# Kernel tuning notes

Hardware: AMD Instinct MI355X
Metric: run time of the kernel (lower is better)

The kernel has to match this reference:

```python
import jax, jax.numpy as jnp
import numpy as np

# --- static config (matches init_kwargs) ---
T, V, D, H = 4096, 32000, 1024, 16
DH = D // H                      # rope/head dim = 64
E, CAP, K, HOPS = 8, 1024, 2, 3  # non-identity experts, capacity, top-k, hops
MLP = 4 * D
ROPE_BASE = 10000.0
ATTN_IDX = np.array([0, 2, 4, 6])  # experts built with i%2==0 -> Attention
FFN_IDX = np.array([1, 3, 5, 7])   # i%2==1 -> FeedForward
EPS = 1e-6


def rope_cos_sin(t, dh, base):
    inv = 1.0 / (base ** (jnp.arange(0, dh, 2, dtype=jnp.float32) / dh))
    ang = jnp.arange(t, dtype=jnp.float32)[:, None] * inv[None, :]  # [T, dh/2]
    ang = jnp.concatenate([ang, ang], axis=-1)                      # [T, dh]
    return jnp.cos(ang), jnp.sin(ang)


def rotate_half(x):
    h = x.shape[-1] // 2
    return jnp.concatenate([-x[..., h:], x[..., :h]], axis=-1)


def topk_mask(logits, k):
    # boolean [T, E_total] mask of per-row top-k
    _, idx = jax.lax.top_k(logits, k)
    hard = jax.nn.one_hot(idx, logits.shape[-1]).sum(axis=-2)
    return hard.astype(bool)


def capacity_select(mask_te, gate_te, capacity):
    # mask_te: [T,E] bool, gate_te: [T,E] float -> slot [E,C,T], kept [E,T]
    m = mask_te.T                                   # [E, T]
    g = jnp.where(m, gate_te.T, -jnp.inf)           # [E, T]
    cap = int(min(capacity, g.shape[1]))
    _, top_idx = jax.lax.top_k(g, cap)              # [E, C]
    Ee, C = top_idx.shape
    slot = jnp.zeros((Ee, C, g.shape[1]), g.dtype)
    slot = slot.at[jnp.arange(Ee)[:, None], jnp.arange(C)[None, :], top_idx].set(1.0)
    slot = slot * m[:, None, :]                     # drop -inf fill slots
    kept = slot.sum(1).astype(bool)                 # [E, T]
    return slot, kept


def rms_norm(x, w):
    return x * jax.lax.rsqrt(jnp.mean(x * x, axis=-1, keepdims=True) + EPS) * w


def attention_group(x, cos_r, sin_r, wq, wk, wv, wo):
    # x: [G,C,D]; cos_r/sin_r: [G,C,DH]; weights: [G,D,D]
    G, C, _ = x.shape
    q = jnp.einsum('gcd,gde->gce', x, wq).reshape(G, C, H, DH)
    k = jnp.einsum('gcd,gde->gce', x, wk).reshape(G, C, H, DH)
    v = jnp.einsum('gcd,gde->gce', x, wv).reshape(G, C, H, DH)
    c = cos_r[:, :, None, :]
    s = sin_r[:, :, None, :]
    q = q * c + rotate_half(q) * s
    k = k * c + rotate_half(k) * s
    scores = jnp.einsum('gqhd,gkhd->ghqk', q, k) / np.sqrt(DH).astype(np.float32)
    attn = jax.nn.softmax(scores, axis=-1)
    out = jnp.einsum('ghqk,gkhd->gqhd', attn, v).reshape(G, C, D)
    return jnp.einsum('gcd,gde->gce', out, wo)


def ffn_group(x, w1, w2):
    # x: [G,C,D]; w1: [G,D,MLP]; w2: [G,MLP,D]
    return jnp.einsum('gcf,gfd->gcd', jax.nn.gelu(jnp.einsum('gcd,gdf->gcf', x, w1)), w2)


def dna_forward(ids, embed_w, router_w, wq, wk, wv, wo, w1, w2, ln_w):
    h = embed_w[ids]                                     # [T, D]
    cos, sin = rope_cos_sin(T, DH, ROPE_BASE)            # [T, DH]
    for hop in range(HOPS):
        logits = h @ router_w[hop].T                     # [T, E+1]
        probs = jax.nn.softmax(logits, axis=-1)
        mask_full = topk_mask(logits, K)                 # [T, E+1]
        probs_tr = probs[:, :-1]                         # [T, E]
        mask_tr = mask_full[:, :-1]
        slot, kept = capacity_select(mask_tr, probs_tr, CAP)  # [E,C,T], [E,T]
        # dispatch
        xin = jnp.einsum('ect,td->ecd', slot, h)          # [E, C, D]
        cos_r = jnp.einsum('ect,td->ecd', slot, cos)      # [E, C, DH]
        sin_r = jnp.einsum('ect,td->ecd', slot, sin)
        # grouped expert execution (stacked params, vectorized over group dim)
        attn_out = attention_group(xin[ATTN_IDX], cos_r[ATTN_IDX], sin_r[ATTN_IDX],
                                   wq, wk, wv, wo)        # [4, C, D]
        ffn_out = ffn_group(xin[FFN_IDX], w1, w2)         # [4, C, D]
        expert_out = jnp.zeros((E, CAP, D), h.dtype)
        expert_out = expert_out.at[ATTN_IDX].set(attn_out).at[FFN_IDX].set(ffn_out)
        # combine
        combine_w = jnp.where(kept.T, probs_tr, 0.0)      # [T, E]
        rho = combine_w.sum(axis=1, keepdims=True)        # [T, 1]
        combine = jnp.einsum('ecd,ect,et->td', expert_out, slot, combine_w.T)
        h = h + combine - rho * h
    return rms_norm(h, ln_w)


def setup_inputs() -> dict:
    key = jax.random.key(0)
    ks = jax.random.split(key, 10)
    sc = 0.02
    return {
        'ids': jax.random.randint(ks[0], (T,), 0, V),
        'embed_w': jax.random.normal(ks[1], (V, D), jnp.float32) * sc,
        'router_w': jax.random.normal(ks[2], (HOPS, E + 1, D), jnp.float32) * sc,
        'wq': jax.random.normal(ks[3], (4, D, D), jnp.float32) * sc,
        'wk': jax.random.normal(ks[4], (4, D, D), jnp.float32) * sc,
        'wv': jax.random.normal(ks[5], (4, D, D), jnp.float32) * sc,
        'wo': jax.random.normal(ks[6], (4, D, D), jnp.float32) * sc,
        'w1': jax.random.normal(ks[7], (4, D, MLP), jnp.float32) * sc,
        'w2': jax.random.normal(ks[8], (4, MLP, D), jnp.float32) * sc,
        'ln_w': jnp.ones((D,), jnp.float32),
    }


def reference(ids, embed_w, router_w, wq, wk, wv, wo, w1, w2, ln_w):
    return dna_forward(ids, embed_w, router_w, wq, wk, wv, wo, w1, w2, ln_w)
```

## Files before the change

### kernel.cpp

```cpp
#include <hip/hip_runtime.h>
#include <math.h>

#define T_ 4096
#define D_ 1024
#define H_ 16
#define DH_ 64
#define E_ 8
#define CAP_ 1024
#define MLP_ 4096
#define HOPS_ 3

__global__ __launch_bounds__(256) void embed_kernel(
    const int* __restrict__ ids, const float* __restrict__ ew, float* __restrict__ h)
{
  const int t = blockIdx.x;
  const int id = ids[t];
  const int c = threadIdx.x * 4;
  *(float4*)(h + (size_t)t * D_ + c) = *(const float4*)(ew + (size_t)id * D_ + c);
}

__global__ __launch_bounds__(64) void router_kernel(
    const float* __restrict__ h, const float* __restrict__ rw,
    float* __restrict__ probs, float* __restrict__ gmask)
{
  const int t = blockIdx.x;
  const int lane = threadIdx.x;
  __shared__ float hs[D_];
  #pragma unroll
  for (int j = 0; j < 4; ++j)
    *(float4*)&hs[lane * 4 + j * 256] = *(const float4*)(h + (size_t)t * D_ + lane * 4 + j * 256);
  __syncthreads();
  float l9[9];
  #pragma unroll
  for (int e = 0; e < 9; ++e) {
    float s = 0.0f;
    for (int i = lane; i < D_; i += 64) s += hs[i] * rw[e * D_ + i];
    #pragma unroll
    for (int off = 32; off > 0; off >>= 1) s += __shfl_down(s, off);
    l9[e] = s;
  }
  if (lane == 0) {
    float m = l9[0];
    #pragma unroll
    for (int e = 1; e < 9; ++e) m = fmaxf(m, l9[e]);
    float sum = 0.0f;
    float ex[9];
    #pragma unroll
    for (int e = 0; e < 9; ++e) { ex[e] = expf(l9[e] - m); sum += ex[e]; }
    const float inv = 1.0f / sum;
    int b1 = 0;
    #pragma unroll
    for (int e = 1; e < 9; ++e) if (l9[e] > l9[b1]) b1 = e;
    int b2 = (b1 == 0) ? 1 : 0;
    #pragma unroll
    for (int e = 0; e < 9; ++e) if (e != b1 && e != b2 && l9[e] > l9[b2]) b2 = e;
    #pragma unroll
    for (int e = 0; e < 8; ++e) {
      const float pe = ex[e] * inv;
      probs[t * 8 + e] = pe;
      gmask[(size_t)e * T_ + t] = (e == b1 || e == b2) ? pe : -1e30f;
    }
  }
}

__global__ __launch_bounds__(256) void zero_kernel(float* __restrict__ rho, int* __restrict__ cnt)
{
  const int i = blockIdx.x * 256 + threadIdx.x;
  if (i < T_) rho[i] = 0.0f;
  if (i < E_) cnt[i] = 0;
}

__global__ __launch_bounds__(256) void select_kernel(
    const float* __restrict__ gmask, const float* __restrict__ probs,
    int* __restrict__ idx, int* __restrict__ cnt, float* __restrict__ rho)
{
  __shared__ float row[T_];
  const int e = blockIdx.y;
  const int tid = threadIdx.x;
  const float* gr = gmask + (size_t)e * T_;
  #pragma unroll
  for (int j = 0; j < 16; ++j) row[tid + 256 * j] = gr[tid + 256 * j];
  __syncthreads();
  const int t = blockIdx.x * 256 + tid;
  const float g = row[t];
  if (g > -1e29f) {
    int rank = 0;
    for (int tt = 0; tt < T_; ++tt) {
      const float gg = row[tt];
      rank += (gg > g) || (gg == g && tt < t);
    }
    if (rank < CAP_) {
      const int pos = atomicAdd(&cnt[e], 1);
      idx[e * CAP_ + pos] = t;
      atomicAdd(&rho[t], probs[t * 8 + e]);
    }
  }
}

__global__ __launch_bounds__(256) void gather_kernel(
    const float* __restrict__ h, const int* __restrict__ idx, const int* __restrict__ cnt,
    float* __restrict__ xin)
{
  const int c = blockIdx.x, e = blockIdx.y;
  const int c4 = threadIdx.x * 4;
  float4* dst = (float4*)(xin + ((size_t)e * CAP_ + c) * D_ + c4);
  if (c < cnt[e]) {
    const int t = idx[e * CAP_ + c];
    *dst = *(const float4*)(h + (size_t)t * D_ + c4);
  } else {
    float4 z; z.x = z.y = z.z = z.w = 0.0f;
    *dst = z;
  }
}

typedef __bf16 bf16x8 __attribute__((ext_vector_type(8)));
typedef float f32x4v __attribute__((ext_vector_type(4)));

union FragU { uint2 u2[2]; bf16x8 v; };

__device__ __forceinline__ unsigned pack_hi2(unsigned u0, unsigned u1)
{
  return (u0 >> 16) | (u1 & 0xFFFF0000u);
}

__device__ __forceinline__ void split8(const float4 a, const float4 b, FragU& h, FragU& l)
{
  const float f[8] = {a.x, a.y, a.z, a.w, b.x, b.y, b.z, b.w};
  unsigned hu[8], lu[8];
  #pragma unroll
  for (int i = 0; i < 8; ++i) {
    const unsigned u = __float_as_uint(f[i]);
    const float lo = f[i] - __uint_as_float(u & 0xFFFF0000u);
    hu[i] = u; lu[i] = __float_as_uint(lo);
  }
  h.u2[0].x = pack_hi2(hu[0], hu[1]); h.u2[0].y = pack_hi2(hu[2], hu[3]);
  h.u2[1].x = pack_hi2(hu[4], hu[5]); h.u2[1].y = pack_hi2(hu[6], hu[7]);
  l.u2[0].x = pack_hi2(lu[0], lu[1]); l.u2[0].y = pack_hi2(lu[2], lu[3]);
  l.u2[1].x = pack_hi2(lu[4], lu[5]); l.u2[1].y = pack_hi2(lu[6], lu[7]);
}

#define BM 128
#define BN 128
#define BK 32
#define LDT 36

__device__ __forceinline__ float gelu_tanh(float x)
{
  const float x3 = x * x * x;
  return 0.5f * x * (1.0f + tanhf(0.7978845608028654f * (x + 0.044715f * x3)));
}

template <int EPI>
__device__ __forceinline__ void gemm_core(
    const float* __restrict__ A, const float* __restrict__ B, float* __restrict__ C,
    int N, int K)
{
  __shared__ unsigned short Ah[BM * LDT];
  __shared__ unsigned short Al[BM * LDT];
  __shared__ unsigned short Bh[BN * LDT];
  __shared__ unsigned short Bl[BN * LDT];

  const int tid = threadIdx.x;
  const int lane = tid & 63;
  const int w = tid >> 6;
  const int wm = w >> 1, wn = w & 1;
  const int m0 = blockIdx.y * BM;
  const int n0 = blockIdx.x * BN;
  const int q = lane >> 4;
  const int l15 = lane & 15;

  const int a_mo = tid >> 3;
  const int a_kq = (tid & 7) * 4;
  const int b_n = tid & 127;
  const int b_kh = (tid >> 7) * 16;

  f32x4v acc[4][4];
  #pragma unroll
  for (int i = 0; i < 4; ++i)
    #pragma unroll
    for (int j = 0; j < 4; ++j) { acc[i][j][0] = 0.f; acc[i][j][1] = 0.f; acc[i][j][2] = 0.f; acc[i][j][3] = 0.f; }

  float4 a_reg[4];
  float b_reg[16];

  const int nk = K / BK;
  #pragma unroll
  for (int t = 0; t < 4; ++t)
    a_reg[t] = *(const float4*)(A + (size_t)(m0 + t * 32 + a_mo) * K + a_kq);
  {
    const float* Bp = B + (size_t)b_kh * N + n0 + b_n;
    #pragma unroll
    for (int i = 0; i < 16; ++i) b_reg[i] = Bp[(size_t)i * N];
  }

  for (int kt = 0; kt < nk; ++kt) {
    __syncthreads();
    #pragma unroll
    for (int t = 0; t < 4; ++t) {
      const int m = t * 32 + a_mo;
      const unsigned u0 = __float_as_uint(a_reg[t].x);
      const unsigned u1 = __float_as_uint(a_reg[t].y);
      const unsigned u2 = __float_as_uint(a_reg[t].z);
      const unsigned u3 = __float_as_uint(a_reg[t].w);
      const float l0 = a_reg[t].x - __uint_as_float(u0 & 0xFFFF0000u);
      const float l1 = a_reg[t].y - __uint_as_float(u1 & 0xFFFF0000u);
      const float l2 = a_reg[t].z - __uint_as_float(u2 & 0xFFFF0000u);
      const float l3 = a_reg[t].w - __uint_as_float(u3 & 0xFFFF0000u);
      uint2 hp, lp;
      hp.x = pack_hi2(u0, u1); hp.y = pack_hi2(u2, u3);
      lp.x = pack_hi2(__float_as_uint(l0), __float_as_uint(l1));
      lp.y = pack_hi2(__float_as_uint(l2), __float_as_uint(l3));
      *(uint2*)&Ah[m * LDT + a_kq] = hp;
      *(uint2*)&Al[m * LDT + a_kq] = lp;
    }
    #pragma unroll
    for (int i = 0; i < 4; ++i) {
      const float f0 = b_reg[4 * i + 0], f1 = b_reg[4 * i + 1];
      const float f2 = b_reg[4 * i + 2], f3 = b_reg[4 * i + 3];
      const unsigned u0 = __float_as_uint(f0);
      const unsigned u1 = __float_as_uint(f1);
      const unsigned u2 = __float_as_uint(f2);
      const unsigned u3 = __float_as_uint(f3);
      const float l0 = f0 - __uint_as_float(u0 & 0xFFFF0000u);
      const float l1 = f1 - __uint_as_float(u1 & 0xFFFF0000u);
      const float l2 = f2 - __uint_as_float(u2 & 0xFFFF0000u);
      const float l3 = f3 - __uint_as_float(u3 & 0xFFFF0000u);
      uint2 hp, lp;
      hp.x = pack_hi2(u0, u1); hp.y = pack_hi2(u2, u3);
      lp.x = pack_hi2(__float_as_uint(l0), __float_as_uint(l1));
      lp.y = pack_hi2(__float_as_uint(l2), __float_as_uint(l3));
      *(uint2*)&Bh[b_n * LDT + b_kh + 4 * i] = hp;
      *(uint2*)&Bl[b_n * LDT + b_kh + 4 * i] = lp;
    }
    if (kt + 1 < nk) {
      const int k0 = (kt + 1) * BK;
      #pragma unroll
      for (int t = 0; t < 4; ++t)
        a_reg[t] = *(const float4*)(A + (size_t)(m0 + t * 32 + a_mo) * K + k0 + a_kq);
      const float* Bp = B + (size_t)(k0 + b_kh) * N + n0 + b_n;
      #pragma unroll
      for (int i = 0; i < 16; ++i) b_reg[i] = Bp[(size_t)i * N];
    }
    __syncthreads();
    FragU fa_h[4], fa_l[4], fb_h[4], fb_l[4];
    #pragma unroll
    for (int i = 0; i < 4; ++i) {
      const int m = wm * 64 + i * 16 + l15;
      const unsigned short* pa = &Ah[m * LDT + q * 8];
      const unsigned short* pl = &Al[m * LDT + q * 8];
      fa_h[i].u2[0] = *(const uint2*)pa; fa_h[i].u2[1] = *(const uint2*)(pa + 4);
      fa_l[i].u2[0] = *(const uint2*)pl; fa_l[i].u2[1] = *(const uint2*)(pl + 4);
    }
    #pragma unroll
    for (int j = 0; j < 4; ++j) {
      const int n = wn * 64 + j * 16 + l15;
      const unsigned short* pb = &Bh[n * LDT + q * 8];
      const unsigned short* pl = &Bl[n * LDT + q * 8];
      fb_h[j].u2[0] = *(const uint2*)pb; fb_h[j].u2[1] = *(const uint2*)(pb + 4);
      fb_l[j].u2[0] = *(const uint2*)pl; fb_l[j].u2[1] = *(const uint2*)(pl + 4);
    }
    #pragma unroll
    for (int i = 0; i < 4; ++i)
      #pragma unroll
      for (int j = 0; j < 4; ++j) {
        acc[i][j] = __builtin_amdgcn_mfma_f32_16x16x32_bf16(fa_h[i].v, fb_h[j].v, acc[i][j], 0, 0, 0);
        acc[i][j] = __builtin_amdgcn_mfma_f32_16x16x32_bf16(fa_h[i].v, fb_l[j].v, acc[i][j], 0, 0, 0);
        acc[i][j] = __builtin_amdgcn_mfma_f32_16x16x32_bf16(fa_l[i].v, fb_h[j].v, acc[i][j], 0, 0, 0);
      }
  }
  #pragma unroll
  for (int i = 0; i < 4; ++i)
    #pragma unroll
    for (int j = 0; j < 4; ++j) {
      const int n = n0 + wn * 64 + j * 16 + l15;
      #pragma unroll
      for (int r = 0; r < 4; ++r) {
        const int m = m0 + wm * 64 + i * 16 + q * 4 + r;
        float v = acc[i][j][r];
        if (EPI == 1) v = gelu_tanh(v);
        C[(size_t)m * N + n] = v;
      }
    }
}

template <int EPI>
__global__ __launch_bounds__(256, 2) void gemm_split(
    const float* __restrict__ Abase, const float* __restrict__ Bbase, float* __restrict__ Cbase,
    int N, int K, long sA, long sB, long sC)
{
  const float* A = Abase + (size_t)blockIdx.z * (size_t)sA;
  const float* B = Bbase + (size_t)blockIdx.z * (size_t)sB;
  float* C = Cbase + (size_t)blockIdx.z * (size_t)sC;
  gemm_core<EPI>(A, B, C, N, K);
}

__global__ __launch_bounds__(256, 2) void gemm_qkv(
    const float* __restrict__ xin,
    const float* __restrict__ wq, const float* __restrict__ wk, const float* __restrict__ wv,
    float* __restrict__ qb, float* __restrict__ kb, float* __restrict__ vb)
{
  const int z = blockIdx.z;
  const int g = z & 3;
  const int which = z >> 2;
  const float* A = xin + (size_t)g * 2 * CAP_ * D_;
  const float* B = ((which == 0) ? wq : (which == 1) ? wk : wv) + (size_t)g * D_ * D_;
  float* C = ((which == 0) ? qb : (which == 1) ? kb : vb) + (size_t)g * CAP_ * D_;
  gemm_core<0>(A, B, C, D_, D_);
}

__global__ __launch_bounds__(256) void rope_kernel(
    float* __restrict__ q, float* __restrict__ k,
    const int* __restrict__ idx, const int* __restrict__ cnt)
{
  const int c = blockIdx.x, g = blockIdx.y;
  const int e = 2 * g;
  if (c >= cnt[e]) return;
  const int t = idx[e * CAP_ + c];
  const int tid = threadIdx.x;
  const int hh = tid >> 4;
  const int pp = tid & 15;
  const size_t base = ((size_t)g * CAP_ + c) * D_ + hh * DH_;
  const float tf = (float)t;
  #pragma unroll
  for (int u = 0; u < 2; ++u) {
    const int i = pp * 2 + u;
    const float invf = (float)::pow(10000.0, -(double)i / 32.0);
    const float ang = tf * invf;
    const float cs = (float)::cos((double)ang);
    const float sn = (float)::sin((double)ang);
    const float q0 = q[base + i], q1 = q[base + i + 32];
    q[base + i]      = q0 * cs - q1 * sn;
    q[base + i + 32] = q1 * cs + q0 * sn;
    const float k0 = k[base + i], k1 = k[base + i + 32];
    k[base + i]      = k0 * cs - k1 * sn;
    k[base + i + 32] = k1 * cs + k0 * sn;
  }
}

#define FBQ 128
#define LDK 68
#define LDQ 72

__global__ __launch_bounds__(256, 2) void flash_mfma(
    const float* __restrict__ qg, const float* __restrict__ kg,
    const float* __restrict__ vg, float* __restrict__ og)
{
  const int g = blockIdx.z, hh = blockIdx.y, qt = blockIdx.x;
  const size_t base = (size_t)g * CAP_ * D_ + hh * DH_;
  const float* Q = qg + base;
  const float* Kp = kg + base;
  const float* Vp = vg + base;
  float* O = og + base;

  __shared__ __align__(16) char lds_raw[69632];
  unsigned short* Kh  = (unsigned short*)lds_raw;
  unsigned short* Kl  = Kh  + 64 * LDK;
  unsigned short* Vth = Kl  + 64 * LDK;
  unsigned short* Vtl = Vth + 64 * LDK;
  unsigned short* Ph  = Vtl + 64 * LDK;
  unsigned short* Pl  = Ph  + FBQ * LDK;
  float* Qs = (float*)lds_raw;

  const int tid = threadIdx.x;
  const int lane = tid & 63;
  const int w = tid >> 6;
  const int quad = lane >> 4;
  const int l15 = lane & 15;

  #pragma unroll
  for (int it = 0; it < 8; ++it) {
    const int row = it * 16 + (tid >> 4);
    const int c4 = (tid & 15) * 4;
    *(float4*)&Qs[row * LDQ + c4] = *(const float4*)(Q + (size_t)(qt * FBQ + row) * D_ + c4);
  }
  __syncthreads();
  FragU qf[2][2][2];
  #pragma unroll
  for (int rs = 0; rs < 2; ++rs)
    #pragma unroll
    for (int ks = 0; ks < 2; ++ks) {
      const float* p0 = &Qs[(w * 32 + rs * 16 + l15) * LDQ + ks * 32 + quad * 8];
      const float4 f0 = *(const float4*)p0;
      const float4 f1 = *(const float4*)(p0 + 4);
      split8(f0, f1, qf[rs][ks][0], qf[rs][ks][1]);
    }
  __syncthreads();

  f32x4v acc[2][4];
  float m_r[2][4], l_r[2][4];
  #pragma unroll
  for (int rs = 0; rs < 2; ++rs)
    #pragma unroll
    for (int r = 0; r < 4; ++r) { m_r[rs][r] = -1e30f; l_r[rs][r] = 0.0f; }
  #pragma unroll
  for (int rs = 0; rs < 2; ++rs)
    #pragma unroll
    for (int dt = 0; dt < 4; ++dt) { acc[rs][dt][0] = 0.f; acc[rs][dt][1] = 0.f; acc[rs][dt][2] = 0.f; acc[rs][dt][3] = 0.f; }

  for (int kt = 0; kt < 16; ++kt) {
    __syncthreads();
    #pragma unroll
    for (int it = 0; it < 4; ++it) {
      const int r = it * 16 + (tid >> 4);
      const int c4 = (tid & 15) * 4;
      const float4 kv = *(const float4*)(Kp + (size_t)(kt * 64 + r) * D_ + c4);
      {
        const unsigned u0 = __float_as_uint(kv.x), u1 = __float_as_uint(kv.y);
        const unsigned u2 = __float_as_uint(kv.z), u3 = __float_as_uint(kv.w);
        const float l0 = kv.x - __uint_as_float(u0 & 0xFFFF0000u);
        const float l1 = kv.y - __uint_as_float(u1 & 0xFFFF0000u);
        const float l2 = kv.z - __uint_as_float(u2 & 0xFFFF0000u);
        const float l3 = kv.w - __uint_as_float(u3 & 0xFFFF0000u);
        uint2 hp, lp;
        hp.x = pack_hi2(u0, u1); hp.y = pack_hi2(u2, u3);
        lp.x = pack_hi2(__float_as_uint(l0), __float_as_uint(l1));
        lp.y = pack_hi2(__float_as_uint(l2), __float_as_uint(l3));
        *(uint2*)&Kh[r * LDK + c4] = hp;
        *(uint2*)&Kl[r * LDK + c4] = lp;
      }
      const float4 vv = *(const float4*)(Vp + (size_t)(kt * 64 + r) * D_ + c4);
      const float vf[4] = {vv.x, vv.y, vv.z, vv.w};
      #pragma unroll
      for (int u = 0; u < 4; ++u) {
        const unsigned uu = __float_as_uint(vf[u]);
        const float lo = vf[u] - __uint_as_float(uu & 0xFFFF0000u);
        Vth[(c4 + u) * LDK + r] = (unsigned short)(uu >> 16);
        Vtl[(c4 + u) * LDK + r] = (unsigned short)(__float_as_uint(lo) >> 16);
      }
    }
    __syncthreads();
    f32x4v sfr[2][4];
    #pragma unroll
    for (int rs = 0; rs < 2; ++rs)
      #pragma unroll
      for (int j = 0; j < 4; ++j) {
        f32x4v s; s[0] = 0.f; s[1] = 0.f; s[2] = 0.f; s[3] = 0.f;
        #pragma unroll
        for (int ks = 0; ks < 2; ++ks) {
          FragU kh, kl;
          const unsigned short* pk = &Kh[(j * 16 + l15) * LDK + ks * 32 + quad * 8];
          const unsigned short* pl = &Kl[(j * 16 + l15) * LDK + ks * 32 + quad * 8];
          kh.u2[0] = *(const uint2*)pk; kh.u2[1] = *(const uint2*)(pk + 4);
          kl.u2[0] = *(const uint2*)pl; kl.u2[1] = *(const uint2*)(pl + 4);
          s = __builtin_amdgcn_mfma_f32_16x16x32_bf16(qf[rs][ks][0].v, kh.v, s, 0, 0, 0);
          s = __builtin_amdgcn_mfma_f32_16x16x32_bf16(qf[rs][ks][0].v, kl.v, s, 0, 0, 0);
          s = __builtin_amdgcn_mfma_f32_16x16x32_bf16(qf[rs][ks][1].v, kh.v, s, 0, 0, 0);
        }
        sfr[rs][j] = s;
      }
    #pragma unroll
    for (int rs = 0; rs < 2; ++rs) {
      #pragma unroll
      for (int r = 0; r < 4; ++r) {
        float s0 = sfr[rs][0][r] * 0.125f;
        float s1 = sfr[rs][1][r] * 0.125f;
        float s2 = sfr[rs][2][r] * 0.125f;
        float s3 = sfr[rs][3][r] * 0.125f;
        float mx = fmaxf(fmaxf(s0, s1), fmaxf(s2, s3));
        #pragma unroll
        for (int o = 1; o < 16; o <<= 1) mx = fmaxf(mx, __shfl_xor(mx, o));
        const float nm = fmaxf(m_r[rs][r], mx);
        const float al = __expf(m_r[rs][r] - nm);
        m_r[rs][r] = nm;
        const float p0 = __expf(s0 - nm);
        const float p1 = __expf(s1 - nm);
        const float p2 = __expf(s2 - nm);
        const float p3 = __expf(s3 - nm);
        float rsum = p0 + p1 + p2 + p3;
        #pragma unroll
        for (int o = 1; o < 16; o <<= 1) rsum += __shfl_xor(rsum, o);
        l_r[rs][r] = l_r[rs][r] * al + rsum;
        #pragma unroll
        for (int dt = 0; dt < 4; ++dt) acc[rs][dt][r] *= al;
        const int row = w * 32 + rs * 16 + quad * 4 + r;
        const float pv[4] = {p0, p1, p2, p3};
        #pragma unroll
        for (int j = 0; j < 4; ++j) {
          const unsigned u = __float_as_uint(pv[j]);
          const float lo = pv[j] - __uint_as_float(u & 0xFFFF0000u);
          Ph[row * LDK + j * 16 + l15] = (unsigned short)(u >> 16);
          Pl[row * LDK + j * 16 + l15] = (unsigned short)(__float_as_uint(lo) >> 16);
        }
      }
    }
    __syncthreads();
    FragU pf[2][2][2];
    #pragma unroll
    for (int rs = 0; rs < 2; ++rs)
      #pragma unroll
      for (int ks = 0; ks < 2; ++ks) {
        const unsigned short* ph = &Ph[(w * 32 + rs * 16 + l15) * LDK + ks * 32 + quad * 8];
        const unsigned short* pl = &Pl[(w * 32 + rs * 16 + l15) * LDK + ks * 32 + quad * 8];
        pf[rs][ks][0].u2[0] = *(const uint2*)ph; pf[rs][ks][0].u2[1] = *(const uint2*)(ph + 4);
        pf[rs][ks][1].u2[0] = *(const uint2*)pl; pf[rs][ks][1].u2[1] = *(const uint2*)(pl + 4);
      }
    #pragma unroll
    for (int dt = 0; dt < 4; ++dt)
      #pragma unroll
      for (int ks = 0; ks < 2; ++ks) {
        FragU vh, vl;
        const unsigned short* pv_ = &Vth[(dt * 16 + l15) * LDK + ks * 32 + quad * 8];
        const unsigned short* pl_ = &Vtl[(dt * 16 + l15) * LDK + ks * 32 + quad * 8];
        vh.u2[0] = *(const uint2*)pv_; vh.u2[1] = *(const uint2*)(pv_ + 4);
        vl.u2[0] = *(const uint2*)pl_; vl.u2[1] = *(const uint2*)(pl_ + 4);
        #pragma unroll
        for (int rs = 0; rs < 2; ++rs) {
          acc[rs][dt] = __builtin_amdgcn_mfma_f32_16x16x32_bf16(pf[rs][ks][0].v, vh.v, acc[rs][dt], 0, 0, 0);
          acc[rs][dt] = __builtin_amdgcn_mfma_f32_16x16x32_bf16(pf[rs][ks][0].v, vl.v, acc[rs][dt], 0, 0, 0);
          acc[rs][dt] = __builtin_amdgcn_mfma_f32_16x16x32_bf16(pf[rs][ks][1].v, vh.v, acc[rs][dt], 0, 0, 0);
        }
      }
  }
  #pragma unroll
  for (int rs = 0; rs < 2; ++rs)
    #pragma unroll
    for (int r = 0; r < 4; ++r) {
      const float inv = 1.0f / l_r[rs][r];
      const int row = qt * FBQ + w * 32 + rs * 16 + quad * 4 + r;
      #pragma unroll
      for (int dt = 0; dt < 4; ++dt)
        O[(size_t)row * D_ + dt * 16 + l15] = acc[rs][dt][r] * inv;
    }
}

__global__ __launch_bounds__(256) void initnew_kernel(
    const float* __restrict__ h, const float* __restrict__ rho, float* __restrict__ hn)
{
  const int t = blockIdx.x;
  const float f = 1.0f - rho[t];
  const int c = threadIdx.x * 4;
  float4 x = *(const float4*)(h + (size_t)t * D_ + c);
  x.x *= f; x.y *= f; x.z *= f; x.w *= f;
  *(float4*)(hn + (size_t)t * D_ + c) = x;
}

__global__ __launch_bounds__(256) void scatter_kernel(
    const float* __restrict__ eo, const int* __restrict__ idx, const int* __restrict__ cnt,
    const float* __restrict__ probs, float* __restrict__ hn)
{
  const int c = blockIdx.x, e = blockIdx.y;
  if (c >= cnt[e]) return;
  const int t = idx[e * CAP_ + c];
  const float w = probs[t * 8 + e];
  const float* src = eo + ((size_t)e * CAP_ + c) * D_;
  float* dst = hn + (size_t)t * D_;
  const int c4 = threadIdx.x * 4;
  #pragma unroll
  for (int j = 0; j < 4; ++j) atomicAdd(dst + c4 + j, src[c4 + j] * w);
}

__global__ __launch_bounds__(256) void rms_kernel(
    const float* __restrict__ h, const float* __restrict__ w, float* __restrict__ out)
{
  const int t = blockIdx.x;
  const int c = threadIdx.x * 4;
  const float4 x = *(const float4*)(h + (size_t)t * D_ + c);
  float ss = x.x * x.x + x.y * x.y + x.z * x.z + x.w * x.w;
  #pragma unroll
  for (int off = 32; off > 0; off >>= 1) ss += __shfl_down(ss, off);
  __shared__ float wsum[4];
  __shared__ float sscale;
  const int lane = threadIdx.x & 63, wv = threadIdx.x >> 6;
  if (lane == 0) wsum[wv] = ss;
  __syncthreads();
  if (threadIdx.x == 0) {
    const float s = wsum[0] + wsum[1] + wsum[2] + wsum[3];
    sscale = 1.0f / sqrtf(s * (1.0f / (float)D_) + 1e-6f);
  }
  __syncthreads();
  const float sc = sscale;
  const float4 w4 = *(const float4*)(w + c);
  float4 o;
  o.x = x.x * sc * w4.x; o.y = x.y * sc * w4.y; o.z = x.z * sc * w4.z; o.w = x.w * sc * w4.w;
  *(float4*)(out + (size_t)t * D_ + c) = o;
}

extern "C" void kernel_launch(void* const* d_in, const int* in_sizes, int n_in,
                              void* d_out, int out_size, void* d_ws, size_t ws_size,
                              hipStream_t stream)
{
  (void)in_sizes; (void)n_in; (void)out_size; (void)ws_size;
  const int* ids = (const int*)d_in[0];
  const float* embed_w = (const float*)d_in[1];
  const float* router_w = (const float*)d_in[2];
  const float* wq = (const float*)d_in[3];
  const float* wk = (const float*)d_in[4];
  const float* wv = (const float*)d_in[5];
  const float* wo = (const float*)d_in[6];
  const float* w1 = (const float*)d_in[7];
  const float* w2 = (const float*)d_in[8];
  const float* lnw = (const float*)d_in[9];
  float* out = (float*)d_out;

  float* p = (float*)d_ws;
  const size_t TD = (size_t)T_ * D_;
  float* hA = p;    p += TD;
  float* hB = p;    p += TD;
  float* probs = p; p += (size_t)T_ * E_;
  float* gmask = p; p += (size_t)E_ * T_;
  float* rho = p;   p += T_;
  int* idx = (int*)p;   p += E_ * CAP_;
  int* cnt = (int*)p;   p += 16;
  float* xin = p;  p += (size_t)E_ * CAP_ * D_;
  float* qb = p;   p += (size_t)4 * CAP_ * D_;
  float* kb = p;   p += (size_t)4 * CAP_ * D_;
  float* vb = p;   p += (size_t)4 * CAP_ * D_;
  float* ao = p;   p += (size_t)4 * CAP_ * D_;
  float* eo = p;   p += (size_t)E_ * CAP_ * D_;
  float* mid = qb;

  embed_kernel<<<T_, 256, 0, stream>>>(ids, embed_w, hA);
  float* cur = hA;
  float* nxt = hB;
  for (int hop = 0; hop < HOPS_; ++hop) {
    router_kernel<<<T_, 64, 0, stream>>>(cur, router_w + (size_t)hop * 9 * D_, probs, gmask);
    zero_kernel<<<16, 256, 0, stream>>>(rho, cnt);
    select_kernel<<<dim3(16, 8), 256, 0, stream>>>(gmask, probs, idx, cnt, rho);
    gather_kernel<<<dim3(CAP_, E_), 256, 0, stream>>>(cur, idx, cnt, xin);
    gemm_qkv<<<dim3(D_ / BN, CAP_ / BM, 12), 256, 0, stream>>>(xin, wq, wk, wv, qb, kb, vb);
    rope_kernel<<<dim3(CAP_, 4), 256, 0, stream>>>(qb, kb, idx, cnt);
    flash_mfma<<<dim3(CAP_ / FBQ, 16, 4), 256, 0, stream>>>(qb, kb, vb, ao);
    gemm_split<0><<<dim3(D_ / BN, CAP_ / BM, 4), 256, 0, stream>>>(
        ao, wo, eo, D_, D_,
        (long)CAP_ * D_, (long)D_ * D_, (long)2 * CAP_ * D_);
    gemm_split<1><<<dim3(MLP_ / BN, CAP_ / BM, 4), 256, 0, stream>>>(
        xin + (size_t)CAP_ * D_, w1, mid, MLP_, D_,
        (long)2 * CAP_ * D_, (long)D_ * MLP_, (long)CAP_ * MLP_);
    gemm_split<0><<<dim3(D_ / BN, CAP_ / BM, 4), 256, 0, stream>>>(
        mid, w2, eo + (size_t)CAP_ * D_, D_, MLP_,
        (long)CAP_ * MLP_, (long)MLP_ * D_, (long)2 * CAP_ * D_);
    initnew_kernel<<<T_, 256, 0, stream>>>(cur, rho, nxt);
    scatter_kernel<<<dim3(CAP_, E_), 256, 0, stream>>>(eo, idx, cnt, probs, nxt);
    float* tmp = cur; cur = nxt; nxt = tmp;
  }
  rms_kernel<<<T_, 256, 0, stream>>>(cur, lnw, out);
}
```

Measured before the change: 2.758 ms.

## Pre-split operands into bf16 hi/lo layout and use direct-to-LDS GEMM loads

Weights are converted once per call into transposed bf16 hi/lo split buffers. Activations (gathered inputs, attention output, GELU output) are written directly in the same split layout. The GEMM core no longer splits fp32 values in its inner loop; it streams pre-split tiles via global_load_lds and runs the three hi/lo product phases as separate K-steps. The wo and w2 GEMMs use split-K with atomicAdd into a zeroed buffer to add parallelism, at the cost of extra conversion passes, atomics, and more workspace.

```diff
diff --git a/kernel.cpp b/kernel.cpp
--- a/kernel.cpp
+++ b/kernel.cpp
@@ -68,6 +68,13 @@
   const int i = blockIdx.x * 256 + threadIdx.x;
   if (i < T_) rho[i] = 0.0f;
   if (i < E_) cnt[i] = 0;
+}
+
+__global__ __launch_bounds__(256) void zeroeo_kernel(float* __restrict__ eo)
+{
+  const size_t i = ((size_t)blockIdx.x * 256 + threadIdx.x) * 4;
+  float4 z; z.x = z.y = z.z = z.w = 0.0f;
+  *(float4*)(eo + i) = z;
 }
 
 __global__ __launch_bounds__(256) void select_kernel(
@@ -97,22 +104,6 @@
   }
 }
 
-__global__ __launch_bounds__(256) void gather_kernel(
-    const float* __restrict__ h, const int* __restrict__ idx, const int* __restrict__ cnt,
-    float* __restrict__ xin)
-{
-  const int c = blockIdx.x, e = blockIdx.y;
-  const int c4 = threadIdx.x * 4;
-  float4* dst = (float4*)(xin + ((size_t)e * CAP_ + c) * D_ + c4);
-  if (c < cnt[e]) {
-    const int t = idx[e * CAP_ + c];
-    *dst = *(const float4*)(h + (size_t)t * D_ + c4);
-  } else {
-    float4 z; z.x = z.y = z.z = z.w = 0.0f;
-    *dst = z;
-  }
-}
-
 typedef __bf16 bf16x8 __attribute__((ext_vector_type(8)));
 typedef float f32x4v __attribute__((ext_vector_type(4)));
 
@@ -139,10 +130,12 @@
   l.u2[1].x = pack_hi2(lu[4], lu[5]); l.u2[1].y = pack_hi2(lu[6], lu[7]);
 }
 
-#define BM 128
-#define BN 128
-#define BK 32
-#define LDT 36
+__device__ __forceinline__ void lds_load16(const void* g, void* l)
+{
+  __builtin_amdgcn_global_load_lds(
+      (const __attribute__((address_space(1))) unsigned int*)g,
+      (__attribute__((address_space(3))) unsigned int*)l, 16, 0, 0);
+}
 
 __device__ __forceinline__ float gelu_tanh(float x)
 {
@@ -150,29 +143,77 @@
   return 0.5f * x * (1.0f + tanhf(0.7978845608028654f * (x + 0.044715f * x3)));
 }
 
+__global__ __launch_bounds__(256) void gather_kernel(
+    const float* __restrict__ h, const int* __restrict__ idx, const int* __restrict__ cnt,
+    unsigned short* __restrict__ xinp)
+{
+  const int c = blockIdx.x, e = blockIdx.y;
+  const int c4 = threadIdx.x * 4;
+  unsigned short* dst = xinp + ((size_t)e * CAP_ + c) * 2 * D_;
+  if (c < cnt[e]) {
+    const int t = idx[e * CAP_ + c];
+    const float4 x = *(const float4*)(h + (size_t)t * D_ + c4);
+    const float f[4] = {x.x, x.y, x.z, x.w};
+    unsigned hu[4], lu[4];
+    #pragma unroll
+    for (int j = 0; j < 4; ++j) {
+      const unsigned u = __float_as_uint(f[j]);
+      const float lo = f[j] - __uint_as_float(u & 0xFFFF0000u);
+      hu[j] = u; lu[j] = __float_as_uint(lo);
+    }
+    uint2 hp, lp;
+    hp.x = pack_hi2(hu[0], hu[1]); hp.y = pack_hi2(hu[2], hu[3]);
+    lp.x = pack_hi2(lu[0], lu[1]); lp.y = pack_hi2(lu[2], lu[3]);
+    *(uint2*)(dst + c4) = hp;
+    *(uint2*)(dst + D_ + c4) = lp;
+  } else {
+    uint2 z; z.x = 0u; z.y = 0u;
+    *(uint2*)(dst + c4) = z;
+    *(uint2*)(dst + D_ + c4) = z;
+  }
+}
+
+__global__ __launch_bounds__(256) void convw_kernel(
+    const float* __restrict__ W, unsigned short* __restrict__ out, int K, int N)
+{
+  const float* Wp = W + (size_t)blockIdx.z * K * N;
+  unsigned short* op = out + (size_t)blockIdx.z * N * 2 * K;
+  const int k0 = blockIdx.y * 64, n0 = blockIdx.x * 64;
+  __shared__ float tile[64][65];
+  const int tr = threadIdx.x >> 6;
+  const int tc = threadIdx.x & 63;
+  #pragma unroll
+  for (int it = 0; it < 16; ++it) {
+    const int r = it * 4 + tr;
+    tile[r][tc] = Wp[(size_t)(k0 + r) * N + n0 + tc];
+  }
+  __syncthreads();
+  #pragma unroll
+  for (int it = 0; it < 16; ++it) {
+    const int n = it * 4 + tr;
+    const float f = tile[tc][n];
+    const unsigned u = __float_as_uint(f);
+    const float lo = f - __uint_as_float(u & 0xFFFF0000u);
+    op[(size_t)(n0 + n) * 2 * K + k0 + tc] = (unsigned short)(u >> 16);
+    op[(size_t)(n0 + n) * 2 * K + K + k0 + tc] = (unsigned short)(__float_as_uint(lo) >> 16);
+  }
+}
+
 template <int EPI>
-__device__ __forceinline__ void gemm_core(
-    const float* __restrict__ A, const float* __restrict__ B, float* __restrict__ C,
-    int N, int K)
-{
-  __shared__ unsigned short Ah[BM * LDT];
-  __shared__ unsigned short Al[BM * LDT];
-  __shared__ unsigned short Bh[BN * LDT];
-  __shared__ unsigned short Bl[BN * LDT];
+__device__ __forceinline__ void gemm_bf16_core(
+    const unsigned short* __restrict__ A, const unsigned short* __restrict__ B,
+    void* __restrict__ Cv, int N, int K, int vt0, int nvt)
+{
+  __shared__ unsigned short As[128 * 64];
+  __shared__ unsigned short Bs[128 * 64];
 
   const int tid = threadIdx.x;
   const int lane = tid & 63;
   const int w = tid >> 6;
   const int wm = w >> 1, wn = w & 1;
-  const int m0 = blockIdx.y * BM;
-  const int n0 = blockIdx.x * BN;
-  const int q = lane >> 4;
-  const int l15 = lane & 15;
-
-  const int a_mo = tid >> 3;
-  const int a_kq = (tid & 7) * 4;
-  const int b_n = tid & 127;
-  const int b_kh = (tid >> 7) * 16;
+  const int quad = lane >> 4, l15 = lane & 15;
+  const int m0 = blockIdx.y * 128, n0 = blockIdx.x * 128;
+  const size_t K2 = (size_t)2 * K;
 
   f32x4v acc[4][4];
   #pragma unroll
@@ -180,94 +221,45 @@
     #pragma unroll
     for (int j = 0; j < 4; ++j) { acc[i][j][0] = 0.f; acc[i][j][1] = 0.f; acc[i][j][2] = 0.f; acc[i][j][3] = 0.f; }
 
-  float4 a_reg[4];
-  float b_reg[16];
-
-  const int nk = K / BK;
-  #pragma unroll
-  for (int t = 0; t < 4; ++t)
-    a_reg[t] = *(const float4*)(A + (size_t)(m0 + t * 32 + a_mo) * K + a_kq);
-  {
-    const float* Bp = B + (size_t)b_kh * N + n0 + b_n;
-    #pragma unroll
-    for (int i = 0; i < 16; ++i) b_reg[i] = Bp[(size_t)i * N];
-  }
-
-  for (int kt = 0; kt < nk; ++kt) {
+  const int r0 = tid >> 3;
+  const int c0 = (tid & 7) * 8;
+
+  for (int vt = vt0; vt < vt0 + nvt; ++vt) {
+    const int kk = vt / 3;
+    const int ph = vt - kk * 3;
+    const int ka = kk * 64 + (ph == 2 ? K : 0);
+    const int kb = kk * 64 + (ph == 1 ? K : 0);
     __syncthreads();
-    #pragma unroll
-    for (int t = 0; t < 4; ++t) {
-      const int m = t * 32 + a_mo;
-      const unsigned u0 = __float_as_uint(a_reg[t].x);
-      const unsigned u1 = __float_as_uint(a_reg[t].y);
-      const unsigned u2 = __float_as_uint(a_reg[t].z);
-      const unsigned u3 = __float_as_uint(a_reg[t].w);
-      const float l0 = a_reg[t].x - __uint_as_float(u0 & 0xFFFF0000u);
-      const float l1 = a_reg[t].y - __uint_as_float(u1 & 0xFFFF0000u);
-      const float l2 = a_reg[t].z - __uint_as_float(u2 & 0xFFFF0000u);
-      const float l3 = a_reg[t].w - __uint_as_float(u3 & 0xFFFF0000u);
-      uint2 hp, lp;
-      hp.x = pack_hi2(u0, u1); hp.y = pack_hi2(u2, u3);
-      lp.x = pack_hi2(__float_as_uint(l0), __float_as_uint(l1));
-      lp.y = pack_hi2(__float_as_uint(l2), __float_as_uint(l3));
-      *(uint2*)&Ah[m * LDT + a_kq] = hp;
-      *(uint2*)&Al[m * LDT + a_kq] = lp;
-    }
-    #pragma unroll
-    for (int i = 0; i < 4; ++i) {
-      const float f0 = b_reg[4 * i + 0], f1 = b_reg[4 * i + 1];
-      const float f2 = b_reg[4 * i + 2], f3 = b_reg[4 * i + 3];
-      const unsigned u0 = __float_as_uint(f0);
-      const unsigned u1 = __float_as_uint(f1);
-      const unsigned u2 = __float_as_uint(f2);
-      const unsigned u3 = __float_as_uint(f3);
-      const float l0 = f0 - __uint_as_float(u0 & 0xFFFF0000u);
-      const float l1 = f1 - __uint_as_float(u1 & 0xFFFF0000u);
-      const float l2 = f2 - __uint_as_float(u2 & 0xFFFF0000u);
-      const float l3 = f3 - __uint_as_float(u3 & 0xFFFF0000u);
-      uint2 hp, lp;
-      hp.x = pack_hi2(u0, u1); hp.y = pack_hi2(u2, u3);
-      lp.x = pack_hi2(__float_as_uint(l0), __float_as_uint(l1));
-      lp.y = pack_hi2(__float_as_uint(l2), __float_as_uint(l3));
-      *(uint2*)&Bh[b_n * LDT + b_kh + 4 * i] = hp;
-      *(uint2*)&Bl[b_n * LDT + b_kh + 4 * i] = lp;
-    }
-    if (kt + 1 < nk) {
-      const int k0 = (kt + 1) * BK;
-      #pragma unroll
-      for (int t = 0; t < 4; ++t)
-        a_reg[t] = *(const float4*)(A + (size_t)(m0 + t * 32 + a_mo) * K + k0 + a_kq);
-      const float* Bp = B + (size_t)(k0 + b_kh) * N + n0 + b_n;
-      #pragma unroll
-      for (int i = 0; i < 16; ++i) b_reg[i] = Bp[(size_t)i * N];
-    }
+    const unsigned short* Ag = A + (size_t)(m0 + r0) * K2 + ka + c0;
+    const unsigned short* Bg = B + (size_t)(n0 + r0) * K2 + kb + c0;
+    #pragma unroll
+    for (int i = 0; i < 4; ++i)
+      lds_load16(Ag + (size_t)(i * 32) * K2, &As[(tid + i * 256) * 8]);
+    #pragma unroll
+    for (int i = 0; i < 4; ++i)
+      lds_load16(Bg + (size_t)(i * 32) * K2, &Bs[(tid + i * 256) * 8]);
     __syncthreads();
-    FragU fa_h[4], fa_l[4], fb_h[4], fb_l[4];
-    #pragma unroll
-    for (int i = 0; i < 4; ++i) {
-      const int m = wm * 64 + i * 16 + l15;
-      const unsigned short* pa = &Ah[m * LDT + q * 8];
-      const unsigned short* pl = &Al[m * LDT + q * 8];
-      fa_h[i].u2[0] = *(const uint2*)pa; fa_h[i].u2[1] = *(const uint2*)(pa + 4);
-      fa_l[i].u2[0] = *(const uint2*)pl; fa_l[i].u2[1] = *(const uint2*)(pl + 4);
-    }
-    #pragma unroll
-    for (int j = 0; j < 4; ++j) {
-      const int n = wn * 64 + j * 16 + l15;
-      const unsigned short* pb = &Bh[n * LDT + q * 8];
-      const unsigned short* pl = &Bl[n * LDT + q * 8];
-      fb_h[j].u2[0] = *(const uint2*)pb; fb_h[j].u2[1] = *(const uint2*)(pb + 4);
-      fb_l[j].u2[0] = *(const uint2*)pl; fb_l[j].u2[1] = *(const uint2*)(pl + 4);
-    }
-    #pragma unroll
-    for (int i = 0; i < 4; ++i)
+    #pragma unroll
+    for (int ks = 0; ks < 2; ++ks) {
+      FragU fa[4], fb[4];
+      #pragma unroll
+      for (int i = 0; i < 4; ++i) {
+        const unsigned short* pa = &As[(wm * 64 + i * 16 + l15) * 64 + ks * 32 + quad * 8];
+        fa[i].u2[0] = *(const uint2*)pa; fa[i].u2[1] = *(const uint2*)(pa + 4);
+      }
       #pragma unroll
       for (int j = 0; j < 4; ++j) {
-        acc[i][j] = __builtin_amdgcn_mfma_f32_16x16x32_bf16(fa_h[i].v, fb_h[j].v, acc[i][j], 0, 0, 0);
-        acc[i][j] = __builtin_amdgcn_mfma_f32_16x16x32_bf16(fa_h[i].v, fb_l[j].v, acc[i][j], 0, 0, 0);
-        acc[i][j] = __builtin_amdgcn_mfma_f32_16x16x32_bf16(fa_l[i].v, fb_h[j].v, acc[i][j], 0, 0, 0);
-      }
-  }
+        const unsigned short* pb = &Bs[(wn * 64 + j * 16 + l15) * 64 + ks * 32 + quad * 8];
+        fb[j].u2[0] = *(const uint2*)pb; fb[j].u2[1] = *(const uint2*)(pb + 4);
+      }
+      #pragma unroll
+      for (int i = 0; i < 4; ++i)
+        #pragma unroll
+        for (int j = 0; j < 4; ++j)
+          acc[i][j] = __builtin_amdgcn_mfma_f32_16x16x32_bf16(fa[i].v, fb[j].v, acc[i][j], 0, 0, 0);
+    }
+  }
+
   #pragma unroll
   for (int i = 0; i < 4; ++i)
     #pragma unroll
@@ -275,37 +267,54 @@
       const int n = n0 + wn * 64 + j * 16 + l15;
       #pragma unroll
       for (int r = 0; r < 4; ++r) {
-        const int m = m0 + wm * 64 + i * 16 + q * 4 + r;
-        float v = acc[i][j][r];
-        if (EPI == 1) v = gelu_tanh(v);
-        C[(size_t)m * N + n] = v;
-      }
-    }
-}
-
-template <int EPI>
-__global__ __launch_bounds__(256, 2) void gemm_split(
-    const float* __restrict__ Abase, const float* __restrict__ Bbase, float* __restrict__ Cbase,
-    int N, int K, long sA, long sB, long sC)
-{
-  const float* A = Abase + (size_t)blockIdx.z * (size_t)sA;
-  const float* B = Bbase + (size_t)blockIdx.z * (size_t)sB;
-  float* C = Cbase + (size_t)blockIdx.z * (size_t)sC;
-  gemm_core<EPI>(A, B, C, N, K);
-}
-
-__global__ __launch_bounds__(256, 2) void gemm_qkv(
-    const float* __restrict__ xin,
-    const float* __restrict__ wq, const float* __restrict__ wk, const float* __restrict__ wv,
+        const int m = m0 + wm * 64 + i * 16 + quad * 4 + r;
+        const float v = acc[i][j][r];
+        if (EPI == 0) {
+          ((float*)Cv)[(size_t)m * N + n] = v;
+        } else if (EPI == 2) {
+          atomicAdd(&((float*)Cv)[(size_t)m * N + n], v);
+        } else {
+          const float gv = gelu_tanh(v);
+          const unsigned u = __float_as_uint(gv);
+          const float lo = gv - __uint_as_float(u & 0xFFFF0000u);
+          unsigned short* C = (unsigned short*)Cv;
+          C[(size_t)m * 2 * N + n] = (unsigned short)(u >> 16);
+          C[(size_t)m * 2 * N + N + n] = (unsigned short)(__float_as_uint(lo) >> 16);
+        }
+      }
+    }
+}
+
+template <int EPI, int SK>
+__global__ __launch_bounds__(256, 2) void gemm_bf16_k(
+    const unsigned short* __restrict__ Ab, const unsigned short* __restrict__ Bb,
+    void* __restrict__ Cb, int N, int K, long sA, long sB, long sC)
+{
+  const int z = blockIdx.z;
+  const int g = z / SK, sp = z - g * SK;
+  const unsigned short* A = Ab + (size_t)g * sA;
+  const unsigned short* B = Bb + (size_t)g * sB;
+  void* C;
+  if (EPI == 1) C = (void*)((unsigned short*)Cb + (size_t)g * sC);
+  else          C = (void*)((float*)Cb + (size_t)g * sC);
+  const int kps = K / 64;
+  const int per = 3 * kps / SK;
+  gemm_bf16_core<EPI>(A, B, C, N, K, sp * per, per);
+}
+
+__global__ __launch_bounds__(256, 2) void gemm_qkv_bf16(
+    const unsigned short* __restrict__ xinp,
+    const unsigned short* __restrict__ wqp, const unsigned short* __restrict__ wkp,
+    const unsigned short* __restrict__ wvp,
     float* __restrict__ qb, float* __restrict__ kb, float* __restrict__ vb)
 {
   const int z = blockIdx.z;
   const int g = z & 3;
   const int which = z >> 2;
-  const float* A = xin + (size_t)g * 2 * CAP_ * D_;
-  const float* B = ((which == 0) ? wq : (which == 1) ? wk : wv) + (size_t)g * D_ * D_;
+  const unsigned short* A = xinp + (size_t)(2 * g) * CAP_ * 2 * D_;
+  const unsigned short* B = ((which == 0) ? wqp : (which == 1) ? wkp : wvp) + (size_t)g * D_ * 2 * D_;
   float* C = ((which == 0) ? qb : (which == 1) ? kb : vb) + (size_t)g * CAP_ * D_;
-  gemm_core<0>(A, B, C, D_, D_);
+  gemm_bf16_core<0>(A, B, (void*)C, D_, D_, 0, 48);
 }
 
 __global__ __launch_bounds__(256) void rope_kernel(
@@ -343,14 +352,14 @@
 
 __global__ __launch_bounds__(256, 2) void flash_mfma(
     const float* __restrict__ qg, const float* __restrict__ kg,
-    const float* __restrict__ vg, float* __restrict__ og)
+    const float* __restrict__ vg, unsigned short* __restrict__ og)
 {
   const int g = blockIdx.z, hh = blockIdx.y, qt = blockIdx.x;
   const size_t base = (size_t)g * CAP_ * D_ + hh * DH_;
   const float* Q = qg + base;
   const float* Kp = kg + base;
   const float* Vp = vg + base;
-  float* O = og + base;
+  unsigned short* Ob = og + (size_t)g * CAP_ * 2 * D_ + hh * DH_;
 
   __shared__ __align__(16) char lds_raw[69632];
   unsigned short* Kh  = (unsigned short*)lds_raw;
@@ -518,8 +527,13 @@
       const float inv = 1.0f / l_r[rs][r];
       const int row = qt * FBQ + w * 32 + rs * 16 + quad * 4 + r;
       #pragma unroll
-      for (int dt = 0; dt < 4; ++dt)
-        O[(size_t)row * D_ + dt * 16 + l15] = acc[rs][dt][r] * inv;
+      for (int dt = 0; dt < 4; ++dt) {
+        const float v = acc[rs][dt][r] * inv;
+        const unsigned u = __float_as_uint(v);
+        const float lo = v - __uint_as_float(u & 0xFFFF0000u);
+        Ob[(size_t)row * 2 * D_ + dt * 16 + l15] = (unsigned short)(u >> 16);
+        Ob[(size_t)row * 2 * D_ + D_ + dt * 16 + l15] = (unsigned short)(__float_as_uint(lo) >> 16);
+      }
     }
 }
 
@@ -601,13 +615,26 @@
   float* rho = p;   p += T_;
   int* idx = (int*)p;   p += E_ * CAP_;
   int* cnt = (int*)p;   p += 16;
-  float* xin = p;  p += (size_t)E_ * CAP_ * D_;
+  float* eo = p;   p += (size_t)E_ * CAP_ * D_;
   float* qb = p;   p += (size_t)4 * CAP_ * D_;
   float* kb = p;   p += (size_t)4 * CAP_ * D_;
   float* vb = p;   p += (size_t)4 * CAP_ * D_;
-  float* ao = p;   p += (size_t)4 * CAP_ * D_;
-  float* eo = p;   p += (size_t)E_ * CAP_ * D_;
-  float* mid = qb;
+  unsigned short* aob = (unsigned short*)p; p += (size_t)4 * CAP_ * D_;
+  unsigned short* midp = (unsigned short*)qb;
+  unsigned short* xinp = (unsigned short*)p; p += (size_t)E_ * CAP_ * D_;
+  unsigned short* wqp = (unsigned short*)p; p += (size_t)4 * D_ * D_;
+  unsigned short* wkp = (unsigned short*)p; p += (size_t)4 * D_ * D_;
+  unsigned short* wvp = (unsigned short*)p; p += (size_t)4 * D_ * D_;
+  unsigned short* wop = (unsigned short*)p; p += (size_t)4 * D_ * D_;
+  unsigned short* w1p = (unsigned short*)p; p += (size_t)4 * D_ * MLP_;
+  unsigned short* w2p = (unsigned short*)p; p += (size_t)4 * D_ * MLP_;
+
+  convw_kernel<<<dim3(D_ / 64, D_ / 64, 4), 256, 0, stream>>>(wq, wqp, D_, D_);
+  convw_kernel<<<dim3(D_ / 64, D_ / 64, 4), 256, 0, stream>>>(wk, wkp, D_, D_);
+  convw_kernel<<<dim3(D_ / 64, D_ / 64, 4), 256, 0, stream>>>(wv, wvp, D_, D_);
+  convw_kernel<<<dim3(D_ / 64, D_ / 64, 4), 256, 0, stream>>>(wo, wop, D_, D_);
+  convw_kernel<<<dim3(MLP_ / 64, D_ / 64, 4), 256, 0, stream>>>(w1, w1p, D_, MLP_);
+  convw_kernel<<<dim3(D_ / 64, MLP_ / 64, 4), 256, 0, stream>>>(w2, w2p, MLP_, D_);
 
   embed_kernel<<<T_, 256, 0, stream>>>(ids, embed_w, hA);
   float* cur = hA;
@@ -616,19 +643,20 @@
     router_kernel<<<T_, 64, 0, stream>>>(cur, router_w + (size_t)hop * 9 * D_, probs, gmask);
     zero_kernel<<<16, 256, 0, stream>>>(rho, cnt);
     select_kernel<<<dim3(16, 8), 256, 0, stream>>>(gmask, probs, idx, cnt, rho);
-    gather_kernel<<<dim3(CAP_, E_), 256, 0, stream>>>(cur, idx, cnt, xin);
-    gemm_qkv<<<dim3(D_ / BN, CAP_ / BM, 12), 256, 0, stream>>>(xin, wq, wk, wv, qb, kb, vb);
+    gather_kernel<<<dim3(CAP_, E_), 256, 0, stream>>>(cur, idx, cnt, xinp);
+    gemm_qkv_bf16<<<dim3(D_ / 128, CAP_ / 128, 12), 256, 0, stream>>>(xinp, wqp, wkp, wvp, qb, kb, vb);
     rope_kernel<<<dim3(CAP_, 4), 256, 0, stream>>>(qb, kb, idx, cnt);
-    flash_mfma<<<dim3(CAP_ / FBQ, 16, 4), 256, 0, stream>>>(qb, kb, vb, ao);
-    gemm_split<0><<<dim3(D_ / BN, CAP_ / BM, 4), 256, 0, stream>>>(
-        ao, wo, eo, D_, D_,
-        (long)CAP_ * D_, (long)D_ * D_, (long)2 * CAP_ * D_);
-    gemm_split<1><<<dim3(MLP_ / BN, CAP_ / BM, 4), 256, 0, stream>>>(
-        xin + (size_t)CAP_ * D_, w1, mid, MLP_, D_,
-        (long)2 * CAP_ * D_, (long)D_ * MLP_, (long)CAP_ * MLP_);
-    gemm_split<0><<<dim3(D_ / BN, CAP_ / BM, 4), 256, 0, stream>>>(
-        mid, w2, eo + (size_t)CAP_ * D_, D_, MLP_,
-        (long)CAP_ * MLP_, (long)MLP_ * D_, (long)2 * CAP_ * D_);
+    flash_mfma<<<dim3(CAP_ / FBQ, 16, 4), 256, 0, stream>>>(qb, kb, vb, aob);
+    zeroeo_kernel<<<8192, 256, 0, stream>>>(eo);
+    gemm_bf16_k<2, 4><<<dim3(D_ / 128, CAP_ / 128, 16), 256, 0, stream>>>(
+        aob, wop, (void*)eo, D_, D_,
+        (long)CAP_ * 2 * D_, (long)D_ * 2 * D_, (long)2 * CAP_ * D_);
+    gemm_bf16_k<1, 1><<<dim3(MLP_ / 128, CAP_ / 128, 4), 256, 0, stream>>>(
+        xinp + (size_t)CAP_ * 2 * D_, w1p, (void*)midp, MLP_, D_,
+        (long)2 * CAP_ * 2 * D_, (long)MLP_ * 2 * D_, (long)CAP_ * 2 * MLP_);
+    gemm_bf16_k<2, 4><<<dim3(D_ / 128, CAP_ / 128, 16), 256, 0, stream>>>(
+        midp, w2p, (void*)(eo + (size_t)CAP_ * D_), D_, MLP_,
+        (long)CAP_ * 2 * MLP_, (long)D_ * 2 * MLP_, (long)2 * CAP_ * D_);
     initnew_kernel<<<T_, 256, 0, stream>>>(cur, rho, nxt);
     scatter_kernel<<<dim3(CAP_, E_), 256, 0, stream>>>(eo, idx, cnt, probs, nxt);
     float* tmp = cur; cur = nxt; nxt = tmp;
```

Result: slower. 3.343 ms (+21.2%).
